# Optimization experiments

Hardware: AMD Instinct MI355X
Metric: run time of the kernel (lower is better)

The kernel has to match this reference:

```python
import jax, jax.numpy as jnp
import numpy as np


def setup_inputs() -> dict:
    key = jax.random.key(0)
    k1, k2 = jax.random.split(key)
    B, N, F = 16, 4096, 512
    S, K = 8, 1024          # splits, symbols per codebook
    D = F // S              # sub-vector dim
    x = jax.random.normal(k1, (B, N, F), dtype=jnp.float32)
    # torch init: uniform(-1/symbols, 1/symbols)
    codebooks = jax.random.uniform(k2, (S, K, D), dtype=jnp.float32,
                                   minval=-1.0 / K, maxval=1.0 / K)
    return {"x": x, "codebooks": codebooks}


def reference(x, codebooks):
    B, N, F = x.shape
    S, K, D = codebooks.shape
    xs = x.reshape(B, N, S, D)                       # split into S chunks
    x2 = jnp.sum(xs * xs, axis=-1, keepdims=True)    # [B,N,S,1]
    c2 = jnp.sum(codebooks * codebooks, axis=-1)     # [S,K]
    xc = jnp.einsum('bnsd,skd->bnsk', xs, codebooks)
    dist = x2 + c2[None, None] - 2.0 * xc            # [B,N,S,K]
    idx = jnp.argmin(dist, axis=-1)                  # [B,N,S]
    # gather chosen code vectors per split -> [B,N,S,D]
    sym = codebooks[jnp.arange(S)[None, None, :], idx]
    sg = jax.lax.stop_gradient
    # straight-through quantized output
    quant = (xs + sg(sym - xs)).reshape(B, N, F)
    # per-split mse (mean over B,N,D of each chunk), summed over splits
    dev = (jnp.sum(jnp.mean((sym - sg(xs)) ** 2, axis=(0, 1, 3)))
           + 0.25 * jnp.sum(jnp.mean((xs - sg(sym)) ** 2, axis=(0, 1, 3))))
    return quant, dev
```

## Files before the change

### kernel.cpp

```cpp
#include <hip/hip_runtime.h>
#include <cstdint>

constexpr int Bv = 16, Nv = 4096, Fv = 512, Sv = 8, Kv = 1024, Dv = 64;
constexpr int Mv = Bv * Nv;
#define BDIM 512
constexpr int RG = 4;

using bf16x8 = __attribute__((ext_vector_type(8))) short;
using f32x4  = __attribute__((ext_vector_type(4))) float;
typedef unsigned short u16;
typedef unsigned int u32;

__device__ __forceinline__ u16 bf16rne(float f) {
  union { float f; u32 u; } v; v.f = f;
  u32 u = v.u + 0x7FFFu + ((v.u >> 16) & 1u);
  return (u16)(u >> 16);
}

__device__ __forceinline__ u32 cvtpk(float lo, float hi) {
  u32 r;
  asm("v_cvt_pk_bf16_f32 %0, %1, %2" : "=v"(r) : "v"(lo), "v"(hi));
  return r;
}

__device__ __forceinline__ void gload_lds16(const void* g, void* lds) {
  __builtin_amdgcn_global_load_lds(
      (const __attribute__((address_space(1))) void*)g,
      (__attribute__((address_space(3))) void*)lds, 16, 0, 0);
}
__device__ __forceinline__ void gload_lds4(const void* g, void* lds) {
  __builtin_amdgcn_global_load_lds(
      (const __attribute__((address_space(1))) void*)g,
      (__attribute__((address_space(3))) void*)lds, 4, 0, 0);
}

__global__ void prep_kernel(const float* __restrict__ cb, u16* __restrict__ swz,
                            float* __restrict__ c2m) {
  int idx = blockIdx.x * 256 + threadIdx.x;
  int cw = idx & (Kv - 1);
  const float4* src = (const float4*)(cb + (size_t)idx * Dv);
  float v[64];
  float s2 = 0.f;
#pragma unroll
  for (int i = 0; i < 16; ++i) {
    float4 f = src[i];
    v[i * 4 + 0] = f.x; v[i * 4 + 1] = f.y; v[i * 4 + 2] = f.z; v[i * 4 + 3] = f.w;
    s2 += f.x * f.x + f.y * f.y + f.z * f.z + f.w * f.w;
  }
  c2m[idx] = -0.5f * s2;
  uint4* out = (uint4*)(swz + (size_t)idx * Dv);
#pragma unroll
  for (int slot = 0; slot < 8; ++slot) {
    int slotp = slot ^ (cw & 7);
    u32 w[4];
#pragma unroll
    for (int p = 0; p < 4; ++p)
      w[p] = (u32)bf16rne(v[slot * 8 + p * 2]) | ((u32)bf16rne(v[slot * 8 + p * 2 + 1]) << 16);
    uint4 pk; pk.x = w[0]; pk.y = w[1]; pk.z = w[2]; pk.w = w[3];
    out[slotp] = pk;
  }
}

__global__ __launch_bounds__(BDIM, 2) void pq_mfma(
    const float* __restrict__ x, const float* __restrict__ cb,
    const u16* __restrict__ swz, const float* __restrict__ c2m_g,
    float* __restrict__ quant, float* __restrict__ devpart) {
  __shared__ __attribute__((aligned(16))) u16 cw_lds[Kv * Dv];
  __shared__ __attribute__((aligned(16))) float c2_lds[Kv];

  const int tid = threadIdx.x;
  const int s = blockIdx.x & 7;
  const int chunk = blockIdx.x >> 3;
  const int wave = tid >> 6, lane = tid & 63;
  const int l15 = lane & 15, lg = lane >> 4;
  const int slotp0 = lg ^ (l15 & 7);
  const int slotp1 = (4 + lg) ^ (l15 & 7);

  const u16* swz_s = swz + (size_t)s * Kv * Dv;
#pragma unroll
  for (int it = 0; it < 16; ++it)
    gload_lds16(swz_s + (size_t)(it * BDIM + tid) * 8,
                &cw_lds[(it * BDIM + (tid & ~63)) * 8]);
#pragma unroll
  for (int it = 0; it < 2; ++it)
    gload_lds4(c2m_g + s * Kv + it * BDIM + tid,
               &c2_lds[it * BDIM + (tid & ~63)]);

  float4 xr[RG][4];
  {
    const float* xb = x + (size_t)(chunk * 1024 + wave * 64) * Fv + s * Dv;
#pragma unroll
    for (int rg = 0; rg < RG; ++rg) {
      const float* xp = xb + (size_t)(rg * 16 + l15) * Fv + lg * 8;
      xr[rg][0] = *(const float4*)xp;
      xr[rg][1] = *(const float4*)(xp + 4);
      xr[rg][2] = *(const float4*)(xp + 32);
      xr[rg][3] = *(const float4*)(xp + 36);
    }
  }

  __syncthreads();

  const u16* r0 = cw_lds + l15 * Dv + slotp0 * 8;
  const u16* r1 = cw_lds + l15 * Dv + slotp1 * 8;

  const u32 lgr0 = (u32)(lg * 4), lgr1 = lgr0 | 1u, lgr2 = lgr0 | 2u, lgr3 = lgr0 | 3u;
  float devx2 = 0.f, bvsum = 0.f;

#pragma unroll 1
  for (int u = 0; u < 2; ++u) {
    const int rowu = chunk * 1024 + u * 512 + wave * 64;

    bf16x8 xf[RG][2];
#pragma unroll
    for (int rg = 0; rg < RG; ++rg) {
#pragma unroll
      for (int h = 0; h < 2; ++h) {
        float4 f0 = xr[rg][h * 2], f1 = xr[rg][h * 2 + 1];
        devx2 += f0.x * f0.x + f0.y * f0.y + f0.z * f0.z + f0.w * f0.w
               + f1.x * f1.x + f1.y * f1.y + f1.z * f1.z + f1.w * f1.w;
        union { u32 w[4]; bf16x8 v; } cvt;
        cvt.w[0] = cvtpk(f0.x, f0.y);
        cvt.w[1] = cvtpk(f0.z, f0.w);
        cvt.w[2] = cvtpk(f1.x, f1.y);
        cvt.w[3] = cvtpk(f1.z, f1.w);
        xf[rg][h] = cvt.v;
      }
    }

    float bv[RG];
#pragma unroll
    for (int rg = 0; rg < RG; ++rg) bv[rg] = -3.0e38f;

    bf16x8 aE0, aE1, aO0, aO1;
    f32x4 c2E, c2O;
    f32x4 accE[RG], accO[RG];

    auto readE = [&](int t) {
      aE0 = *(const bf16x8*)(r0 + t * 16 * Dv);
      aE1 = *(const bf16x8*)(r1 + t * 16 * Dv);
      c2E = *(const f32x4*)&c2_lds[t * 16 + lg * 4];
    };
    auto readO = [&](int t) {
      aO0 = *(const bf16x8*)(r0 + t * 16 * Dv);
      aO1 = *(const bf16x8*)(r1 + t * 16 * Dv);
      c2O = *(const f32x4*)&c2_lds[t * 16 + lg * 4];
    };
    auto mfmaE = [&]() {
      __builtin_amdgcn_s_setprio(1);
#pragma unroll
      for (int rg = 0; rg < RG; ++rg)
        accE[rg] = __builtin_amdgcn_mfma_f32_16x16x32_bf16(aE0, xf[rg][0], c2E, 0, 0, 0);
#pragma unroll
      for (int rg = 0; rg < RG; ++rg)
        accE[rg] = __builtin_amdgcn_mfma_f32_16x16x32_bf16(aE1, xf[rg][1], accE[rg], 0, 0, 0);
      __builtin_amdgcn_s_setprio(0);
    };
    auto mfmaO = [&]() {
      __builtin_amdgcn_s_setprio(1);
#pragma unroll
      for (int rg = 0; rg < RG; ++rg)
        accO[rg] = __builtin_amdgcn_mfma_f32_16x16x32_bf16(aO0, xf[rg][0], c2O, 0, 0, 0);
#pragma unroll
      for (int rg = 0; rg < RG; ++rg)
        accO[rg] = __builtin_amdgcn_mfma_f32_16x16x32_bf16(aO1, xf[rg][1], accO[rg], 0, 0, 0);
      __builtin_amdgcn_s_setprio(0);
    };
    auto procE = [&](int tp) {
      const u32 tb = (u32)(tp << 4);
#pragma unroll
      for (int rg = 0; rg < RG; ++rg) {
        float p0 = __builtin_bit_cast(float, (__builtin_bit_cast(u32, accE[rg][0]) | tb) | lgr0);
        float p1 = __builtin_bit_cast(float, (__builtin_bit_cast(u32, accE[rg][1]) | tb) | lgr1);
        float p2 = __builtin_bit_cast(float, (__builtin_bit_cast(u32, accE[rg][2]) | tb) | lgr2);
        float p3 = __builtin_bit_cast(float, (__builtin_bit_cast(u32, accE[rg][3]) | tb) | lgr3);
        float m = fmaxf(fmaxf(p0, p1), p2);
        bv[rg] = fmaxf(fmaxf(m, p3), bv[rg]);
      }
    };
    auto procO = [&](int tp) {
      const u32 tb = (u32)(tp << 4);
#pragma unroll
      for (int rg = 0; rg < RG; ++rg) {
        float p0 = __builtin_bit_cast(float, (__builtin_bit_cast(u32, accO[rg][0]) | tb) | lgr0);
        float p1 = __builtin_bit_cast(float, (__builtin_bit_cast(u32, accO[rg][1]) | tb) | lgr1);
        float p2 = __builtin_bit_cast(float, (__builtin_bit_cast(u32, accO[rg][2]) | tb) | lgr2);
        float p3 = __builtin_bit_cast(float, (__builtin_bit_cast(u32, accO[rg][3]) | tb) | lgr3);
        float m = fmaxf(fmaxf(p0, p1), p2);
        bv[rg] = fmaxf(fmaxf(m, p3), bv[rg]);
      }
    };

    readE(0);
    mfmaE();
#pragma unroll 1
    for (int t = 1; t < 63; t += 2) {
      readO(t);
      mfmaO();
      procE(t - 1);
      readE(t + 1);
      mfmaE();
      procO(t);
    }
    readO(63);
    mfmaO();
    procE(62);
    procO(63);

#pragma unroll
    for (int rg = 0; rg < RG; ++rg) {
      float b = bv[rg];
      b = fmaxf(b, __shfl_xor(b, 16, 64));
      b = fmaxf(b, __shfl_xor(b, 32, 64));
      bv[rg] = b;
      bvsum += b;
    }

    if (u == 0) {
      const float* xb = x + (size_t)(chunk * 1024 + 512 + wave * 64) * Fv + s * Dv;
#pragma unroll
      for (int rg = 0; rg < RG; ++rg) {
        const float* xp = xb + (size_t)(rg * 16 + l15) * Fv + lg * 8;
        xr[rg][0] = *(const float4*)xp;
        xr[rg][1] = *(const float4*)(xp + 4);
        xr[rg][2] = *(const float4*)(xp + 32);
        xr[rg][3] = *(const float4*)(xp + 36);
      }
    }

    const float* cbs = cb + (size_t)s * Kv * Dv;
    float* qbase = quant + (size_t)rowu * Fv + s * Dv;
#pragma unroll
    for (int i = 0; i < 16; ++i) {
      int rl = i * 4 + lg;
      int kk = __shfl(__builtin_bit_cast(int, bv[i >> 2]), 4 * (i & 3) + lg, 64) & 1023;
      f32x4 v = *(const f32x4*)(cbs + (size_t)kk * Dv + l15 * 4);
      __builtin_nontemporal_store(v, (f32x4*)(qbase + (size_t)rl * Fv + l15 * 4));
    }
  }

#pragma unroll
  for (int m = 1; m <= 32; m <<= 1) devx2 += __shfl_xor(devx2, m, 64);
#pragma unroll
  for (int m = 1; m <= 8; m <<= 1) bvsum += __shfl_xor(bvsum, m, 64);
  if (lane == 0)
    devpart[(size_t)blockIdx.x * 8 + wave] = devx2 - 2.f * bvsum;
}

__global__ void dev_reduce(const float* __restrict__ part, float* __restrict__ out) {
  __shared__ float sred[256];
  int tid = threadIdx.x;
  float s = 0.f;
  for (int i = tid; i < 4096; i += 256) s += part[i];
  sred[tid] = s;
  __syncthreads();
  for (int off = 128; off > 0; off >>= 1) {
    if (tid < off) sred[tid] += sred[tid + off];
    __syncthreads();
  }
  if (tid == 0) out[0] = sred[0] * (1.25f / 4194304.0f);
}

extern "C" void kernel_launch(void* const* d_in, const int* in_sizes, int n_in,
                              void* d_out, int out_size, void* d_ws, size_t ws_size,
                              hipStream_t stream) {
  const float* x = (const float*)d_in[0];
  const float* cb = (const float*)d_in[1];
  float* quant = (float*)d_out;
  float* dev = quant + (size_t)Mv * Fv;

  u16* swz = (u16*)d_ws;
  float* c2m = (float*)(swz + (size_t)Sv * Kv * Dv);
  float* part = c2m + Sv * Kv;

  prep_kernel<<<(Sv * Kv) / 256, 256, 0, stream>>>(cb, swz, c2m);
  pq_mfma<<<512, BDIM, 0, stream>>>(x, cb, swz, c2m, quant, part);
  dev_reduce<<<1, 256, 0, stream>>>(part, dev);
}
```

Baseline: 104.7 us.

## Halve codebook LDS footprint and double grid for higher occupancy

Each block now keeps only half the codebook (512 codes) in LDS at a time, restaging the second half after a barrier, and handles 512 rows instead of 1024. The grid doubles to 1024 blocks and launch bounds ask for 4 blocks per CU, so more waves can hide latency and the load spreads better over the CUs. In exchange each block stages the codebook in two serialized phases with extra barriers, codebook traffic per row doubles, and the register budget per thread shrinks, which may cause spills.

Result: slower. 116.8 us (+11.6%).

```diff
diff --git a/kernel.cpp b/kernel.cpp
--- a/kernel.cpp
+++ b/kernel.cpp
@@ -61,11 +61,11 @@
   }
 }
 
-__global__ __launch_bounds__(BDIM, 2) void pq_mfma(
+__global__ __launch_bounds__(BDIM, 4) void pq_mfma(
     const float* __restrict__ x, const float* __restrict__ cb,
     const u16* __restrict__ swz, const float* __restrict__ c2m_g,
     float* __restrict__ quant, float* __restrict__ devpart) {
-  __shared__ __attribute__((aligned(16))) u16 cw_lds[Kv * Dv];
+  __shared__ __attribute__((aligned(16))) u16 cw_lds[512 * Dv];
   __shared__ __attribute__((aligned(16))) float c2_lds[Kv];
 
   const int tid = threadIdx.x;
@@ -77,18 +77,24 @@
   const int slotp1 = (4 + lg) ^ (l15 & 7);
 
   const u16* swz_s = swz + (size_t)s * Kv * Dv;
-#pragma unroll
-  for (int it = 0; it < 16; ++it)
-    gload_lds16(swz_s + (size_t)(it * BDIM + tid) * 8,
-                &cw_lds[(it * BDIM + (tid & ~63)) * 8]);
-#pragma unroll
+
+  auto stage_half = [&](int h) {
+    const u16* src = swz_s + (size_t)h * (512 * Dv);
+#pragma unroll
+    for (int it = 0; it < 8; ++it)
+      gload_lds16(src + (size_t)(it * BDIM + tid) * 8,
+                  &cw_lds[(it * BDIM + (tid & ~63)) * 8]);
+  };
+
+  #pragma unroll
   for (int it = 0; it < 2; ++it)
     gload_lds4(c2m_g + s * Kv + it * BDIM + tid,
                &c2_lds[it * BDIM + (tid & ~63)]);
+  stage_half(0);
 
   float4 xr[RG][4];
   {
-    const float* xb = x + (size_t)(chunk * 1024 + wave * 64) * Fv + s * Dv;
+    const float* xb = x + (size_t)(chunk * 512 + wave * 64) * Fv + s * Dv;
 #pragma unroll
     for (int rg = 0; rg < RG; ++rg) {
       const float* xp = xb + (size_t)(rg * 16 + l15) * Fv + lg * 8;
@@ -99,144 +105,136 @@
     }
   }
 
+  bf16x8 xf[RG][2];
+  float devx2 = 0.f;
+#pragma unroll
+  for (int rg = 0; rg < RG; ++rg) {
+#pragma unroll
+    for (int h = 0; h < 2; ++h) {
+      float4 f0 = xr[rg][h * 2], f1 = xr[rg][h * 2 + 1];
+      devx2 += f0.x * f0.x + f0.y * f0.y + f0.z * f0.z + f0.w * f0.w
+             + f1.x * f1.x + f1.y * f1.y + f1.z * f1.z + f1.w * f1.w;
+      union { u32 w[4]; bf16x8 v; } cvt;
+      cvt.w[0] = cvtpk(f0.x, f0.y);
+      cvt.w[1] = cvtpk(f0.z, f0.w);
+      cvt.w[2] = cvtpk(f1.x, f1.y);
+      cvt.w[3] = cvtpk(f1.z, f1.w);
+      xf[rg][h] = cvt.v;
+    }
+  }
+
   __syncthreads();
 
   const u16* r0 = cw_lds + l15 * Dv + slotp0 * 8;
   const u16* r1 = cw_lds + l15 * Dv + slotp1 * 8;
 
   const u32 lgr0 = (u32)(lg * 4), lgr1 = lgr0 | 1u, lgr2 = lgr0 | 2u, lgr3 = lgr0 | 3u;
-  float devx2 = 0.f, bvsum = 0.f;
-
-#pragma unroll 1
-  for (int u = 0; u < 2; ++u) {
-    const int rowu = chunk * 1024 + u * 512 + wave * 64;
-
-    bf16x8 xf[RG][2];
+
+  float bv[RG];
+#pragma unroll
+  for (int rg = 0; rg < RG; ++rg) bv[rg] = -3.0e38f;
+
+  bf16x8 aE0, aE1, aO0, aO1;
+  f32x4 c2E, c2O;
+  f32x4 accE[RG], accO[RG];
+
+  auto readE = [&](int h, int t) {
+    aE0 = *(const bf16x8*)(r0 + t * 16 * Dv);
+    aE1 = *(const bf16x8*)(r1 + t * 16 * Dv);
+    c2E = *(const f32x4*)&c2_lds[(h << 9) + t * 16 + lg * 4];
+  };
+  auto readO = [&](int h, int t) {
+    aO0 = *(const bf16x8*)(r0 + t * 16 * Dv);
+    aO1 = *(const bf16x8*)(r1 + t * 16 * Dv);
+    c2O = *(const f32x4*)&c2_lds[(h << 9) + t * 16 + lg * 4];
+  };
+  auto mfmaE = [&]() {
+    __builtin_amdgcn_s_setprio(1);
+#pragma unroll
+    for (int rg = 0; rg < RG; ++rg)
+      accE[rg] = __builtin_amdgcn_mfma_f32_16x16x32_bf16(aE0, xf[rg][0], c2E, 0, 0, 0);
+#pragma unroll
+    for (int rg = 0; rg < RG; ++rg)
+      accE[rg] = __builtin_amdgcn_mfma_f32_16x16x32_bf16(aE1, xf[rg][1], accE[rg], 0, 0, 0);
+    __builtin_amdgcn_s_setprio(0);
+  };
+  auto mfmaO = [&]() {
+    __builtin_amdgcn_s_setprio(1);
+#pragma unroll
+    for (int rg = 0; rg < RG; ++rg)
+      accO[rg] = __builtin_amdgcn_mfma_f32_16x16x32_bf16(aO0, xf[rg][0], c2O, 0, 0, 0);
+#pragma unroll
+    for (int rg = 0; rg < RG; ++rg)
+      accO[rg] = __builtin_amdgcn_mfma_f32_16x16x32_bf16(aO1, xf[rg][1], accO[rg], 0, 0, 0);
+    __builtin_amdgcn_s_setprio(0);
+  };
+  auto procE = [&](u32 tb) {
 #pragma unroll
     for (int rg = 0; rg < RG; ++rg) {
-#pragma unroll
-      for (int h = 0; h < 2; ++h) {
-        float4 f0 = xr[rg][h * 2], f1 = xr[rg][h * 2 + 1];
-        devx2 += f0.x * f0.x + f0.y * f0.y + f0.z * f0.z + f0.w * f0.w
-               + f1.x * f1.x + f1.y * f1.y + f1.z * f1.z + f1.w * f1.w;
-        union { u32 w[4]; bf16x8 v; } cvt;
-        cvt.w[0] = cvtpk(f0.x, f0.y);
-        cvt.w[1] = cvtpk(f0.z, f0.w);
-        cvt.w[2] = cvtpk(f1.x, f1.y);
-        cvt.w[3] = cvtpk(f1.z, f1.w);
-        xf[rg][h] = cvt.v;
-      }
-    }
-
-    float bv[RG];
-#pragma unroll
-    for (int rg = 0; rg < RG; ++rg) bv[rg] = -3.0e38f;
-
-    bf16x8 aE0, aE1, aO0, aO1;
-    f32x4 c2E, c2O;
-    f32x4 accE[RG], accO[RG];
-
-    auto readE = [&](int t) {
-      aE0 = *(const bf16x8*)(r0 + t * 16 * Dv);
-      aE1 = *(const bf16x8*)(r1 + t * 16 * Dv);
-      c2E = *(const f32x4*)&c2_lds[t * 16 + lg * 4];
-    };
-    auto readO = [&](int t) {
-      aO0 = *(const bf16x8*)(r0 + t * 16 * Dv);
-      aO1 = *(const bf16x8*)(r1 + t * 16 * Dv);
-      c2O = *(const f32x4*)&c2_lds[t * 16 + lg * 4];
-    };
-    auto mfmaE = [&]() {
-      __builtin_amdgcn_s_setprio(1);
-#pragma unroll
-      for (int rg = 0; rg < RG; ++rg)
-        accE[rg] = __builtin_amdgcn_mfma_f32_16x16x32_bf16(aE0, xf[rg][0], c2E, 0, 0, 0);
-#pragma unroll
-      for (int rg = 0; rg < RG; ++rg)
-        accE[rg] = __builtin_amdgcn_mfma_f32_16x16x32_bf16(aE1, xf[rg][1], accE[rg], 0, 0, 0);
-      __builtin_amdgcn_s_setprio(0);
-    };
-    auto mfmaO = [&]() {
-      __builtin_amdgcn_s_setprio(1);
-#pragma unroll
-      for (int rg = 0; rg < RG; ++rg)
-        accO[rg] = __builtin_amdgcn_mfma_f32_16x16x32_bf16(aO0, xf[rg][0], c2O, 0, 0, 0);
-#pragma unroll
-      for (int rg = 0; rg < RG; ++rg)
-        accO[rg] = __builtin_amdgcn_mfma_f32_16x16x32_bf16(aO1, xf[rg][1], accO[rg], 0, 0, 0);
-      __builtin_amdgcn_s_setprio(0);
-    };
-    auto procE = [&](int tp) {
-      const u32 tb = (u32)(tp << 4);
-#pragma unroll
-      for (int rg = 0; rg < RG; ++rg) {
-        float p0 = __builtin_bit_cast(float, (__builtin_bit_cast(u32, accE[rg][0]) | tb) | lgr0);
-        float p1 = __builtin_bit_cast(float, (__builtin_bit_cast(u32, accE[rg][1]) | tb) | lgr1);
-        float p2 = __builtin_bit_cast(float, (__builtin_bit_cast(u32, accE[rg][2]) | tb) | lgr2);
-        float p3 = __builtin_bit_cast(float, (__builtin_bit_cast(u32, accE[rg][3]) | tb) | lgr3);
-        float m = fmaxf(fmaxf(p0, p1), p2);
-        bv[rg] = fmaxf(fmaxf(m, p3), bv[rg]);
-      }
-    };
-    auto procO = [&](int tp) {
-      const u32 tb = (u32)(tp << 4);
-#pragma unroll
-      for (int rg = 0; rg < RG; ++rg) {
-        float p0 = __builtin_bit_cast(float, (__builtin_bit_cast(u32, accO[rg][0]) | tb) | lgr0);
-        float p1 = __builtin_bit_cast(float, (__builtin_bit_cast(u32, accO[rg][1]) | tb) | lgr1);
-        float p2 = __builtin_bit_cast(float, (__builtin_bit_cast(u32, accO[rg][2]) | tb) | lgr2);
-        float p3 = __builtin_bit_cast(float, (__builtin_bit_cast(u32, accO[rg][3]) | tb) | lgr3);
-        float m = fmaxf(fmaxf(p0, p1), p2);
-        bv[rg] = fmaxf(fmaxf(m, p3), bv[rg]);
-      }
-    };
-
-    readE(0);
+      float p0 = __builtin_bit_cast(float, (__builtin_bit_cast(u32, accE[rg][0]) | tb) | lgr0);
+      float p1 = __builtin_bit_cast(float, (__builtin_bit_cast(u32, accE[rg][1]) | tb) | lgr1);
+      float p2 = __builtin_bit_cast(float, (__builtin_bit_cast(u32, accE[rg][2]) | tb) | lgr2);
+      float p3 = __builtin_bit_cast(float, (__builtin_bit_cast(u32, accE[rg][3]) | tb) | lgr3);
+      float m = fmaxf(fmaxf(p0, p1), p2);
+      bv[rg] = fmaxf(fmaxf(m, p3), bv[rg]);
+    }
+  };
+  auto procO = [&](u32 tb) {
+#pragma unroll
+    for (int rg = 0; rg < RG; ++rg) {
+      float p0 = __builtin_bit_cast(float, (__builtin_bit_cast(u32, accO[rg][0]) | tb) | lgr0);
+      float p1 = __builtin_bit_cast(float, (__builtin_bit_cast(u32, accO[rg][1]) | tb) | lgr1);
+      float p2 = __builtin_bit_cast(float, (__builtin_bit_cast(u32, accO[rg][2]) | tb) | lgr2);
+      float p3 = __builtin_bit_cast(float, (__builtin_bit_cast(u32, accO[rg][3]) | tb) | lgr3);
+      float m = fmaxf(fmaxf(p0, p1), p2);
+      bv[rg] = fmaxf(fmaxf(m, p3), bv[rg]);
+    }
+  };
+
+  auto kloop = [&](int h) {
+    const u32 hb = (u32)(h << 13);
+    readE(h, 0);
+    readO(h, 1);
     mfmaE();
 #pragma unroll 1
-    for (int t = 1; t < 63; t += 2) {
-      readO(t);
-      mfmaO();
-      procE(t - 1);
-      readE(t + 1);
-      mfmaE();
-      procO(t);
-    }
-    readO(63);
-    mfmaO();
-    procE(62);
-    procO(63);
-
-#pragma unroll
-    for (int rg = 0; rg < RG; ++rg) {
-      float b = bv[rg];
-      b = fmaxf(b, __shfl_xor(b, 16, 64));
-      b = fmaxf(b, __shfl_xor(b, 32, 64));
-      bv[rg] = b;
-      bvsum += b;
-    }
-
-    if (u == 0) {
-      const float* xb = x + (size_t)(chunk * 1024 + 512 + wave * 64) * Fv + s * Dv;
-#pragma unroll
-      for (int rg = 0; rg < RG; ++rg) {
-        const float* xp = xb + (size_t)(rg * 16 + l15) * Fv + lg * 8;
-        xr[rg][0] = *(const float4*)xp;
-        xr[rg][1] = *(const float4*)(xp + 4);
-        xr[rg][2] = *(const float4*)(xp + 32);
-        xr[rg][3] = *(const float4*)(xp + 36);
-      }
-    }
-
-    const float* cbs = cb + (size_t)s * Kv * Dv;
-    float* qbase = quant + (size_t)rowu * Fv + s * Dv;
-#pragma unroll
-    for (int i = 0; i < 16; ++i) {
-      int rl = i * 4 + lg;
-      int kk = __shfl(__builtin_bit_cast(int, bv[i >> 2]), 4 * (i & 3) + lg, 64) & 1023;
-      f32x4 v = *(const f32x4*)(cbs + (size_t)kk * Dv + l15 * 4);
-      __builtin_nontemporal_store(v, (f32x4*)(qbase + (size_t)rl * Fv + l15 * 4));
-    }
+    for (int t = 0; t < 28; t += 2) {
+      readE(h, t + 2); mfmaO(); procE(hb | (u32)(t << 4));
+      readO(h, t + 3); mfmaE(); procO(hb | (u32)((t + 1) << 4));
+    }
+    readE(h, 30); mfmaO(); procE(hb | (28u << 4));
+    readO(h, 31); mfmaE(); procO(hb | (29u << 4));
+    mfmaO(); procE(hb | (30u << 4));
+    procO(hb | (31u << 4));
+  };
+
+  kloop(0);
+
+  __syncthreads();
+  stage_half(1);
+  asm volatile("s_waitcnt vmcnt(0)" ::: "memory");
+  __syncthreads();
+
+  kloop(1);
+
+  float bvsum = 0.f;
+#pragma unroll
+  for (int rg = 0; rg < RG; ++rg) {
+    float b = bv[rg];
+    b = fmaxf(b, __shfl_xor(b, 16, 64));
+    b = fmaxf(b, __shfl_xor(b, 32, 64));
+    bv[rg] = b;
+    bvsum += b;
+  }
+
+  const int rowu = chunk * 512 + wave * 64;
+  const float* cbs = cb + (size_t)s * Kv * Dv;
+  float* qbase = quant + (size_t)rowu * Fv + s * Dv;
+#pragma unroll
+  for (int i = 0; i < 16; ++i) {
+    int rl = i * 4 + lg;
+    int kk = __shfl(__builtin_bit_cast(int, bv[i >> 2]), 4 * (i & 3) + lg, 64) & 1023;
+    f32x4 v = *(const f32x4*)(cbs + (size_t)kk * Dv + l15 * 4);
+    __builtin_nontemporal_store(v, (f32x4*)(qbase + (size_t)rl * Fv + l15 * 4));
   }
 
 #pragma unroll
@@ -251,7 +249,7 @@
   __shared__ float sred[256];
   int tid = threadIdx.x;
   float s = 0.f;
-  for (int i = tid; i < 4096; i += 256) s += part[i];
+  for (int i = tid; i < 8192; i += 256) s += part[i];
   sred[tid] = s;
   __syncthreads();
   for (int off = 128; off > 0; off >>= 1) {
@@ -274,6 +272,6 @@
   float* part = c2m + Sv * Kv;
 
   prep_kernel<<<(Sv * Kv) / 256, 256, 0, stream>>>(cb, swz, c2m);
-  pq_mfma<<<512, BDIM, 0, stream>>>(x, cb, swz, c2m, quant, part);
+  pq_mfma<<<1024, BDIM, 0, stream>>>(x, cb, swz, c2m, quant, part);
   dev_reduce<<<1, 256, 0, stream>>>(part, dev);
 }
```

## Double block size to 16 waves and drop two-pass row loop

Applied to the files above, without the earlier changes.

Blocks grow from 512 to 1024 threads, so each block covers its 1024 rows in a single pass instead of two sequential halves. The outer u loop and the mid-loop reload of x are gone, and the codebook and c2 LDS fill is shared by twice as many waves. The MFMA pipeline is restructured to prefetch two tiles ahead, and the partial-dev buffer and reduction are resized to 16 waves per block. The trade-off is that with launch_bounds(1024,2) each thread gets fewer registers, which risks spills or lower occupancy, and there is no longer any overlap between the x loads and compute.

Result: slower. 121.5 us (+16.1%).

```diff
diff --git a/kernel.cpp b/kernel.cpp
--- a/kernel.cpp
+++ b/kernel.cpp
@@ -3,7 +3,7 @@
 
 constexpr int Bv = 16, Nv = 4096, Fv = 512, Sv = 8, Kv = 1024, Dv = 64;
 constexpr int Mv = Bv * Nv;
-#define BDIM 512
+#define BDIM 1024
 constexpr int RG = 4;
 
 using bf16x8 = __attribute__((ext_vector_type(8))) short;
@@ -78,13 +78,10 @@
 
   const u16* swz_s = swz + (size_t)s * Kv * Dv;
 #pragma unroll
-  for (int it = 0; it < 16; ++it)
+  for (int it = 0; it < 8; ++it)
     gload_lds16(swz_s + (size_t)(it * BDIM + tid) * 8,
                 &cw_lds[(it * BDIM + (tid & ~63)) * 8]);
-#pragma unroll
-  for (int it = 0; it < 2; ++it)
-    gload_lds4(c2m_g + s * Kv + it * BDIM + tid,
-               &c2_lds[it * BDIM + (tid & ~63)]);
+  gload_lds4(c2m_g + s * Kv + tid, &c2_lds[tid & ~63]);
 
   float4 xr[RG][4];
   {
@@ -99,144 +96,124 @@
     }
   }
 
+  bf16x8 xf[RG][2];
+  float devx2 = 0.f;
+#pragma unroll
+  for (int rg = 0; rg < RG; ++rg) {
+#pragma unroll
+    for (int h = 0; h < 2; ++h) {
+      float4 f0 = xr[rg][h * 2], f1 = xr[rg][h * 2 + 1];
+      devx2 += f0.x * f0.x + f0.y * f0.y + f0.z * f0.z + f0.w * f0.w
+             + f1.x * f1.x + f1.y * f1.y + f1.z * f1.z + f1.w * f1.w;
+      union { u32 w[4]; bf16x8 v; } cvt;
+      cvt.w[0] = cvtpk(f0.x, f0.y);
+      cvt.w[1] = cvtpk(f0.z, f0.w);
+      cvt.w[2] = cvtpk(f1.x, f1.y);
+      cvt.w[3] = cvtpk(f1.z, f1.w);
+      xf[rg][h] = cvt.v;
+    }
+  }
+
   __syncthreads();
 
   const u16* r0 = cw_lds + l15 * Dv + slotp0 * 8;
   const u16* r1 = cw_lds + l15 * Dv + slotp1 * 8;
 
   const u32 lgr0 = (u32)(lg * 4), lgr1 = lgr0 | 1u, lgr2 = lgr0 | 2u, lgr3 = lgr0 | 3u;
-  float devx2 = 0.f, bvsum = 0.f;
-
+
+  float bv[RG];
+#pragma unroll
+  for (int rg = 0; rg < RG; ++rg) bv[rg] = -3.0e38f;
+
+  bf16x8 aE0, aE1, aO0, aO1;
+  f32x4 c2E, c2O;
+  f32x4 accE[RG], accO[RG];
+
+  auto readE = [&](int t) {
+    aE0 = *(const bf16x8*)(r0 + t * 16 * Dv);
+    aE1 = *(const bf16x8*)(r1 + t * 16 * Dv);
+    c2E = *(const f32x4*)&c2_lds[t * 16 + lg * 4];
+  };
+  auto readO = [&](int t) {
+    aO0 = *(const bf16x8*)(r0 + t * 16 * Dv);
+    aO1 = *(const bf16x8*)(r1 + t * 16 * Dv);
+    c2O = *(const f32x4*)&c2_lds[t * 16 + lg * 4];
+  };
+  auto mfmaE = [&]() {
+    __builtin_amdgcn_s_setprio(1);
+#pragma unroll
+    for (int rg = 0; rg < RG; ++rg)
+      accE[rg] = __builtin_amdgcn_mfma_f32_16x16x32_bf16(aE0, xf[rg][0], c2E, 0, 0, 0);
+#pragma unroll
+    for (int rg = 0; rg < RG; ++rg)
+      accE[rg] = __builtin_amdgcn_mfma_f32_16x16x32_bf16(aE1, xf[rg][1], accE[rg], 0, 0, 0);
+    __builtin_amdgcn_s_setprio(0);
+  };
+  auto mfmaO = [&]() {
+    __builtin_amdgcn_s_setprio(1);
+#pragma unroll
+    for (int rg = 0; rg < RG; ++rg)
+      accO[rg] = __builtin_amdgcn_mfma_f32_16x16x32_bf16(aO0, xf[rg][0], c2O, 0, 0, 0);
+#pragma unroll
+    for (int rg = 0; rg < RG; ++rg)
+      accO[rg] = __builtin_amdgcn_mfma_f32_16x16x32_bf16(aO1, xf[rg][1], accO[rg], 0, 0, 0);
+    __builtin_amdgcn_s_setprio(0);
+  };
+  auto procE = [&](u32 tb) {
+#pragma unroll
+    for (int rg = 0; rg < RG; ++rg) {
+      float p0 = __builtin_bit_cast(float, (__builtin_bit_cast(u32, accE[rg][0]) | tb) | lgr0);
+      float p1 = __builtin_bit_cast(float, (__builtin_bit_cast(u32, accE[rg][1]) | tb) | lgr1);
+      float p2 = __builtin_bit_cast(float, (__builtin_bit_cast(u32, accE[rg][2]) | tb) | lgr2);
+      float p3 = __builtin_bit_cast(float, (__builtin_bit_cast(u32, accE[rg][3]) | tb) | lgr3);
+      float m = fmaxf(fmaxf(p0, p1), p2);
+      bv[rg] = fmaxf(fmaxf(m, p3), bv[rg]);
+    }
+  };
+  auto procO = [&](u32 tb) {
+#pragma unroll
+    for (int rg = 0; rg < RG; ++rg) {
+      float p0 = __builtin_bit_cast(float, (__builtin_bit_cast(u32, accO[rg][0]) | tb) | lgr0);
+      float p1 = __builtin_bit_cast(float, (__builtin_bit_cast(u32, accO[rg][1]) | tb) | lgr1);
+      float p2 = __builtin_bit_cast(float, (__builtin_bit_cast(u32, accO[rg][2]) | tb) | lgr2);
+      float p3 = __builtin_bit_cast(float, (__builtin_bit_cast(u32, accO[rg][3]) | tb) | lgr3);
+      float m = fmaxf(fmaxf(p0, p1), p2);
+      bv[rg] = fmaxf(fmaxf(m, p3), bv[rg]);
+    }
+  };
+
+  readE(0);
+  readO(1);
+  mfmaE();
 #pragma unroll 1
-  for (int u = 0; u < 2; ++u) {
-    const int rowu = chunk * 1024 + u * 512 + wave * 64;
-
-    bf16x8 xf[RG][2];
-#pragma unroll
-    for (int rg = 0; rg < RG; ++rg) {
-#pragma unroll
-      for (int h = 0; h < 2; ++h) {
-        float4 f0 = xr[rg][h * 2], f1 = xr[rg][h * 2 + 1];
-        devx2 += f0.x * f0.x + f0.y * f0.y + f0.z * f0.z + f0.w * f0.w
-               + f1.x * f1.x + f1.y * f1.y + f1.z * f1.z + f1.w * f1.w;
-        union { u32 w[4]; bf16x8 v; } cvt;
-        cvt.w[0] = cvtpk(f0.x, f0.y);
-        cvt.w[1] = cvtpk(f0.z, f0.w);
-        cvt.w[2] = cvtpk(f1.x, f1.y);
-        cvt.w[3] = cvtpk(f1.z, f1.w);
-        xf[rg][h] = cvt.v;
-      }
-    }
-
-    float bv[RG];
-#pragma unroll
-    for (int rg = 0; rg < RG; ++rg) bv[rg] = -3.0e38f;
-
-    bf16x8 aE0, aE1, aO0, aO1;
-    f32x4 c2E, c2O;
-    f32x4 accE[RG], accO[RG];
-
-    auto readE = [&](int t) {
-      aE0 = *(const bf16x8*)(r0 + t * 16 * Dv);
-      aE1 = *(const bf16x8*)(r1 + t * 16 * Dv);
-      c2E = *(const f32x4*)&c2_lds[t * 16 + lg * 4];
-    };
-    auto readO = [&](int t) {
-      aO0 = *(const bf16x8*)(r0 + t * 16 * Dv);
-      aO1 = *(const bf16x8*)(r1 + t * 16 * Dv);
-      c2O = *(const f32x4*)&c2_lds[t * 16 + lg * 4];
-    };
-    auto mfmaE = [&]() {
-      __builtin_amdgcn_s_setprio(1);
-#pragma unroll
-      for (int rg = 0; rg < RG; ++rg)
-        accE[rg] = __builtin_amdgcn_mfma_f32_16x16x32_bf16(aE0, xf[rg][0], c2E, 0, 0, 0);
-#pragma unroll
-      for (int rg = 0; rg < RG; ++rg)
-        accE[rg] = __builtin_amdgcn_mfma_f32_16x16x32_bf16(aE1, xf[rg][1], accE[rg], 0, 0, 0);
-      __builtin_amdgcn_s_setprio(0);
-    };
-    auto mfmaO = [&]() {
-      __builtin_amdgcn_s_setprio(1);
-#pragma unroll
-      for (int rg = 0; rg < RG; ++rg)
-        accO[rg] = __builtin_amdgcn_mfma_f32_16x16x32_bf16(aO0, xf[rg][0], c2O, 0, 0, 0);
-#pragma unroll
-      for (int rg = 0; rg < RG; ++rg)
-        accO[rg] = __builtin_amdgcn_mfma_f32_16x16x32_bf16(aO1, xf[rg][1], accO[rg], 0, 0, 0);
-      __builtin_amdgcn_s_setprio(0);
-    };
-    auto procE = [&](int tp) {
-      const u32 tb = (u32)(tp << 4);
-#pragma unroll
-      for (int rg = 0; rg < RG; ++rg) {
-        float p0 = __builtin_bit_cast(float, (__builtin_bit_cast(u32, accE[rg][0]) | tb) | lgr0);
-        float p1 = __builtin_bit_cast(float, (__builtin_bit_cast(u32, accE[rg][1]) | tb) | lgr1);
-        float p2 = __builtin_bit_cast(float, (__builtin_bit_cast(u32, accE[rg][2]) | tb) | lgr2);
-        float p3 = __builtin_bit_cast(float, (__builtin_bit_cast(u32, accE[rg][3]) | tb) | lgr3);
-        float m = fmaxf(fmaxf(p0, p1), p2);
-        bv[rg] = fmaxf(fmaxf(m, p3), bv[rg]);
-      }
-    };
-    auto procO = [&](int tp) {
-      const u32 tb = (u32)(tp << 4);
-#pragma unroll
-      for (int rg = 0; rg < RG; ++rg) {
-        float p0 = __builtin_bit_cast(float, (__builtin_bit_cast(u32, accO[rg][0]) | tb) | lgr0);
-        float p1 = __builtin_bit_cast(float, (__builtin_bit_cast(u32, accO[rg][1]) | tb) | lgr1);
-        float p2 = __builtin_bit_cast(float, (__builtin_bit_cast(u32, accO[rg][2]) | tb) | lgr2);
-        float p3 = __builtin_bit_cast(float, (__builtin_bit_cast(u32, accO[rg][3]) | tb) | lgr3);
-        float m = fmaxf(fmaxf(p0, p1), p2);
-        bv[rg] = fmaxf(fmaxf(m, p3), bv[rg]);
-      }
-    };
-
-    readE(0);
-    mfmaE();
-#pragma unroll 1
-    for (int t = 1; t < 63; t += 2) {
-      readO(t);
-      mfmaO();
-      procE(t - 1);
-      readE(t + 1);
-      mfmaE();
-      procO(t);
-    }
-    readO(63);
-    mfmaO();
-    procE(62);
-    procO(63);
-
-#pragma unroll
-    for (int rg = 0; rg < RG; ++rg) {
-      float b = bv[rg];
-      b = fmaxf(b, __shfl_xor(b, 16, 64));
-      b = fmaxf(b, __shfl_xor(b, 32, 64));
-      bv[rg] = b;
-      bvsum += b;
-    }
-
-    if (u == 0) {
-      const float* xb = x + (size_t)(chunk * 1024 + 512 + wave * 64) * Fv + s * Dv;
-#pragma unroll
-      for (int rg = 0; rg < RG; ++rg) {
-        const float* xp = xb + (size_t)(rg * 16 + l15) * Fv + lg * 8;
-        xr[rg][0] = *(const float4*)xp;
-        xr[rg][1] = *(const float4*)(xp + 4);
-        xr[rg][2] = *(const float4*)(xp + 32);
-        xr[rg][3] = *(const float4*)(xp + 36);
-      }
-    }
-
-    const float* cbs = cb + (size_t)s * Kv * Dv;
-    float* qbase = quant + (size_t)rowu * Fv + s * Dv;
-#pragma unroll
-    for (int i = 0; i < 16; ++i) {
-      int rl = i * 4 + lg;
-      int kk = __shfl(__builtin_bit_cast(int, bv[i >> 2]), 4 * (i & 3) + lg, 64) & 1023;
-      f32x4 v = *(const f32x4*)(cbs + (size_t)kk * Dv + l15 * 4);
-      __builtin_nontemporal_store(v, (f32x4*)(qbase + (size_t)rl * Fv + l15 * 4));
-    }
+  for (int t = 0; t < 60; t += 2) {
+    readE(t + 2); mfmaO(); procE((u32)(t << 4));
+    readO(t + 3); mfmaE(); procO((u32)((t + 1) << 4));
+  }
+  readE(62); mfmaO(); procE(60u << 4);
+  readO(63); mfmaE(); procO(61u << 4);
+  mfmaO(); procE(62u << 4);
+  procO(63u << 4);
+
+  float bvsum = 0.f;
+#pragma unroll
+  for (int rg = 0; rg < RG; ++rg) {
+    float b = bv[rg];
+    b = fmaxf(b, __shfl_xor(b, 16, 64));
+    b = fmaxf(b, __shfl_xor(b, 32, 64));
+    bv[rg] = b;
+    bvsum += b;
+  }
+
+  const int rowu = chunk * 1024 + wave * 64;
+  const float* cbs = cb + (size_t)s * Kv * Dv;
+  float* qbase = quant + (size_t)rowu * Fv + s * Dv;
+#pragma unroll
+  for (int i = 0; i < 16; ++i) {
+    int rl = i * 4 + lg;
+    int kk = __shfl(__builtin_bit_cast(int, bv[i >> 2]), 4 * (i & 3) + lg, 64) & 1023;
+    f32x4 v = *(const f32x4*)(cbs + (size_t)kk * Dv + l15 * 4);
+    __builtin_nontemporal_store(v, (f32x4*)(qbase + (size_t)rl * Fv + l15 * 4));
   }
 
 #pragma unroll
@@ -244,14 +221,14 @@
 #pragma unroll
   for (int m = 1; m <= 8; m <<= 1) bvsum += __shfl_xor(bvsum, m, 64);
   if (lane == 0)
-    devpart[(size_t)blockIdx.x * 8 + wave] = devx2 - 2.f * bvsum;
+    devpart[(size_t)blockIdx.x * 16 + wave] = devx2 - 2.f * bvsum;
 }
 
 __global__ void dev_reduce(const float* __restrict__ part, float* __restrict__ out) {
   __shared__ float sred[256];
   int tid = threadIdx.x;
   float s = 0.f;
-  for (int i = tid; i < 4096; i += 256) s += part[i];
+  for (int i = tid; i < 8192; i += 256) s += part[i];
   sred[tid] = s;
   __syncthreads();
   for (int off = 128; off > 0; off >>= 1) {
```
